# Optimization experiments

Hardware: AMD Instinct MI355X
Metric: run time of the kernel (lower is better)

Reference implementation:

```python
import jax, jax.numpy as jnp
import numpy as np

N_NODES = 500000
EMB = 32
K = 10          # sampled neighbors per node (num_sample in source)
BATCH = 100000


def setup_inputs() -> dict:
    key = jax.random.key(0)
    k1, k2, k3, k4, k5 = jax.random.split(key, 5)
    # xavier-ish scale for weights [emb, 2*emb]
    w_scale = jnp.sqrt(2.0 / (EMB + 2 * EMB)).astype(jnp.float32)
    emb = jax.random.normal(k1, (N_NODES, EMB), dtype=jnp.float32)
    W1 = jax.random.normal(k2, (EMB, 2 * EMB), dtype=jnp.float32) * w_scale
    W2 = jax.random.normal(k3, (EMB, 2 * EMB), dtype=jnp.float32) * w_scale
    node_batch = jax.random.randint(k4, (BATCH,), 0, N_NODES)
    neigh = jax.random.randint(k5, (N_NODES, K), 0, N_NODES)
    return {"emb": emb, "W1": W1, "W2": W2,
            "node_batch": node_batch, "neigh": neigh}


def _sage_layer(self_feat, agg_feat, W):
    # SageLayer.forward: relu(W.mm(cat([self, agg], 1).t()).t()) == relu(cat @ W.T)
    combined = jnp.concatenate([self_feat, agg_feat], axis=1)  # [n, 2E]
    return jax.nn.relu(combined @ W.T)                          # [n, E]


def reference(emb, W1, W2, node_batch, neigh):
    # Layer 1: MEAN aggregation of K sampled neighbors for every node
    # (mask.mm(embed_matrix) with row-normalized 0/1 mask == gather + mean)
    agg1 = jnp.take(emb, neigh, axis=0).mean(axis=1)   # [N, E]
    h1 = _sage_layer(emb, agg1, W1)                    # [N, E]
    # Layer 2: aggregate over neighbors of the batch nodes using layer-1 embeds
    nb_neigh = jnp.take(neigh, node_batch, axis=0)     # [B, K]
    agg2 = jnp.take(h1, nb_neigh, axis=0).mean(axis=1) # [B, E]
    out = _sage_layer(jnp.take(h1, node_batch, axis=0), agg2, W2)  # [B, E]
    return out
```

## Files before the change

kernel.cpp:

```cpp
#include <hip/hip_runtime.h>

#define EMBD 32
#define KN 10

__device__ __forceinline__ float bf2f(unsigned short u) {
    union { unsigned int u; float f; } c; c.u = ((unsigned int)u) << 16; return c.f;
}
__device__ __forceinline__ unsigned short f2bf(float f) {
    union { float f; unsigned int u; } c; c.f = f;
    unsigned int u = c.u + 0x7FFFu + ((c.u >> 16) & 1u);
    return (unsigned short)(u >> 16);
}

__global__ __launch_bounds__(256)
void cvt_bf16_kernel(const float4* __restrict__ in, ushort4* __restrict__ out, int n4)
{
    int i = blockIdx.x * 256 + threadIdx.x;
    if (i < n4) {
        float4 v = in[i];
        ushort4 o;
        o.x = f2bf(v.x); o.y = f2bf(v.y); o.z = f2bf(v.z); o.w = f2bf(v.w);
        out[i] = o;
    }
}

template<bool REMAP, bool OUT_BF16>
__global__ __launch_bounds__(256, 4)
void sage_layer(const unsigned short* __restrict__ feat,
                const float* __restrict__ W,
                const int*   __restrict__ neigh,
                const int*   __restrict__ remap,
                void*        __restrict__ out,
                int n_rows)
{
    __shared__ float sh[64][65];
    __shared__ int   s_nb[64][KN];
    __shared__ int   s_node[64];

    const int tid  = threadIdx.x;
    const int row0 = blockIdx.x << 6;

    if constexpr (REMAP) {
        if (tid < 64) {
            int r = row0 + tid;
            if (r >= n_rows) r = n_rows - 1;
            s_node[tid] = remap[r];
        }
        __syncthreads();
    }

    #pragma unroll
    for (int e = tid; e < 64 * KN; e += 256) {
        const int rl = e / KN;
        const int k  = e - rl * KN;
        int node;
        if constexpr (REMAP) {
            node = s_node[rl];
        } else {
            int r = row0 + rl;
            node = (r >= n_rows) ? n_rows - 1 : r;
        }
        s_nb[rl][k] = neigh[node * KN + k];
    }
    __syncthreads();

    {
        const int hw = tid >> 5;
        const int j  = tid & 31;
        #pragma unroll 2
        for (int i = 0; i < 8; ++i) {
            const int rl = hw * 8 + i;
            int node;
            if constexpr (REMAP) {
                node = s_node[rl];
            } else {
                int r = row0 + rl;
                node = (r >= n_rows) ? n_rows - 1 : r;
            }
            const float self = bf2f(feat[node * EMBD + j]);
            float agg = 0.f;
            #pragma unroll
            for (int k = 0; k < KN; ++k)
                agg += bf2f(feat[s_nb[rl][k] * EMBD + j]);
            sh[j][rl]      = self;
            sh[32 + j][rl] = agg * 0.1f;
        }
    }
    __syncthreads();

    const int row = tid & 63;
    const int wid = __builtin_amdgcn_readfirstlane(tid >> 6);
    const float* Wb = W + wid * 8 * 64;

    float acc[8] = {0.f,0.f,0.f,0.f,0.f,0.f,0.f,0.f};
    #pragma unroll 8
    for (int jj = 0; jj < 64; ++jj) {
        const float c = sh[jj][row];
        #pragma unroll
        for (int q = 0; q < 8; ++q)
            acc[q] = fmaf(c, Wb[q * 64 + jj], acc[q]);
    }

    const int r = row0 + row;
    if (r < n_rows) {
        if (OUT_BF16) {
            unsigned int pk[4];
            #pragma unroll
            for (int q = 0; q < 4; ++q) {
                float a0 = fmaxf(acc[2*q],     0.f);
                float a1 = fmaxf(acc[2*q + 1], 0.f);
                pk[q] = (unsigned int)f2bf(a0) | ((unsigned int)f2bf(a1) << 16);
            }
            uint4* dst = (uint4*)((unsigned short*)out + (size_t)r * EMBD + wid * 8);
            *dst = make_uint4(pk[0], pk[1], pk[2], pk[3]);
        } else {
            float* dst = (float*)out + (size_t)r * EMBD + wid * 8;
            ((float4*)dst)[0] = make_float4(fmaxf(acc[0],0.f), fmaxf(acc[1],0.f),
                                            fmaxf(acc[2],0.f), fmaxf(acc[3],0.f));
            ((float4*)dst)[1] = make_float4(fmaxf(acc[4],0.f), fmaxf(acc[5],0.f),
                                            fmaxf(acc[6],0.f), fmaxf(acc[7],0.f));
        }
    }
}

extern "C" void kernel_launch(void* const* d_in, const int* in_sizes, int n_in,
                              void* d_out, int out_size, void* d_ws, size_t ws_size,
                              hipStream_t stream)
{
    const float* emb        = (const float*)d_in[0];
    const float* W1         = (const float*)d_in[1];
    const float* W2         = (const float*)d_in[2];
    const int*   node_batch = (const int*)  d_in[3];
    const int*   neigh      = (const int*)  d_in[4];

    const int N = in_sizes[0] / EMBD;
    const int B = in_sizes[3];

    unsigned short* emb_bf = (unsigned short*)d_ws;
    unsigned short* h1_bf  = emb_bf + (size_t)N * EMBD;

    const int n4 = (N * EMBD) / 4;
    cvt_bf16_kernel<<<(n4 + 255) / 256, 256, 0, stream>>>(
        (const float4*)emb, (ushort4*)emb_bf, n4);

    sage_layer<false, true><<<(N + 63) / 64, 256, 0, stream>>>(
        emb_bf, W1, neigh, nullptr, (void*)h1_bf, N);

    sage_layer<true, false><<<(B + 63) / 64, 256, 0, stream>>>(
        h1_bf, W2, neigh, node_batch, d_out, B);
}
```

Baseline: 232.5 us.

## Split fused SAGE layer into separate gather and GEMM-ReLU kernels

The single kernel that gathered the neighbor mean and did the small GEMM is replaced by two kernels. The first, agg_gather, runs at higher occupancy (launch bounds 256, 8) and writes the bf16 neighbor mean to a workspace buffer. The second, gemm_relu, reads the self features and the stored aggregate and applies W and ReLU. Layer-1 output is written in place over the bf16 embedding buffer. The aim is better latency hiding for the random gathers, at the cost of an extra round trip of the aggregate through global memory, two more launches, and extra bf16 rounding of the aggregate.

```diff
diff --git a/kernel.cpp b/kernel.cpp
--- a/kernel.cpp
+++ b/kernel.cpp
@@ -24,19 +24,16 @@
     }
 }
 
-template<bool REMAP, bool OUT_BF16>
-__global__ __launch_bounds__(256, 4)
-void sage_layer(const unsigned short* __restrict__ feat,
-                const float* __restrict__ W,
-                const int*   __restrict__ neigh,
-                const int*   __restrict__ remap,
-                void*        __restrict__ out,
+template<bool REMAP>
+__global__ __launch_bounds__(256, 8)
+void agg_gather(const unsigned short* __restrict__ feat,
+                const int*            __restrict__ neigh,
+                const int*            __restrict__ remap,
+                unsigned short*       __restrict__ aggout,
                 int n_rows)
 {
-    __shared__ float sh[64][65];
-    __shared__ int   s_nb[64][KN];
-    __shared__ int   s_node[64];
-
+    __shared__ int s_nb[64][KN];
+    __shared__ int s_node[64];
     const int tid  = threadIdx.x;
     const int row0 = blockIdx.x << 6;
 
@@ -54,15 +51,49 @@
         const int rl = e / KN;
         const int k  = e - rl * KN;
         int node;
-        if constexpr (REMAP) {
-            node = s_node[rl];
-        } else {
-            int r = row0 + rl;
-            node = (r >= n_rows) ? n_rows - 1 : r;
-        }
+        if constexpr (REMAP) node = s_node[rl];
+        else { int r = row0 + rl; node = (r >= n_rows) ? n_rows - 1 : r; }
         s_nb[rl][k] = neigh[node * KN + k];
     }
     __syncthreads();
+
+    const int hw = tid >> 5;
+    const int j  = tid & 31;
+    #pragma unroll 2
+    for (int i = 0; i < 8; ++i) {
+        const int rl = hw * 8 + i;
+        const int r  = row0 + rl;
+        float agg = 0.f;
+        #pragma unroll
+        for (int k = 0; k < KN; ++k)
+            agg += bf2f(feat[s_nb[rl][k] * EMBD + j]);
+        if (r < n_rows)
+            aggout[r * EMBD + j] = f2bf(agg * 0.1f);
+    }
+}
+
+template<bool SELF_REMAP, bool OUT_BF16>
+__global__ __launch_bounds__(256, 4)
+void gemm_relu(const unsigned short* __restrict__ selff,
+               const unsigned short* __restrict__ agg,
+               const float*          __restrict__ W,
+               const int*            __restrict__ remap,
+               void*                 __restrict__ out,
+               int n_rows)
+{
+    __shared__ float sh[64][65];
+    __shared__ int   s_node[64];
+    const int tid  = threadIdx.x;
+    const int row0 = blockIdx.x << 6;
+
+    if constexpr (SELF_REMAP) {
+        if (tid < 64) {
+            int r = row0 + tid;
+            if (r >= n_rows) r = n_rows - 1;
+            s_node[tid] = remap[r];
+        }
+        __syncthreads();
+    }
 
     {
         const int hw = tid >> 5;
@@ -70,20 +101,11 @@
         #pragma unroll 2
         for (int i = 0; i < 8; ++i) {
             const int rl = hw * 8 + i;
-            int node;
-            if constexpr (REMAP) {
-                node = s_node[rl];
-            } else {
-                int r = row0 + rl;
-                node = (r >= n_rows) ? n_rows - 1 : r;
-            }
-            const float self = bf2f(feat[node * EMBD + j]);
-            float agg = 0.f;
-            #pragma unroll
-            for (int k = 0; k < KN; ++k)
-                agg += bf2f(feat[s_nb[rl][k] * EMBD + j]);
-            sh[j][rl]      = self;
-            sh[32 + j][rl] = agg * 0.1f;
+            int r = row0 + rl;
+            if (r >= n_rows) r = n_rows - 1;
+            const int node = SELF_REMAP ? s_node[rl] : r;
+            sh[j][rl]      = bf2f(selff[node * EMBD + j]);
+            sh[32 + j][rl] = bf2f(agg[r * EMBD + j]);
         }
     }
     __syncthreads();
@@ -137,15 +159,19 @@
     const int B = in_sizes[3];
 
     unsigned short* emb_bf = (unsigned short*)d_ws;
-    unsigned short* h1_bf  = emb_bf + (size_t)N * EMBD;
+    unsigned short* agg_bf = emb_bf + (size_t)N * EMBD;
 
     const int n4 = (N * EMBD) / 4;
     cvt_bf16_kernel<<<(n4 + 255) / 256, 256, 0, stream>>>(
         (const float4*)emb, (ushort4*)emb_bf, n4);
 
-    sage_layer<false, true><<<(N + 63) / 64, 256, 0, stream>>>(
-        emb_bf, W1, neigh, nullptr, (void*)h1_bf, N);
+    agg_gather<false><<<(N + 63) / 64, 256, 0, stream>>>(
+        emb_bf, neigh, nullptr, agg_bf, N);
+    gemm_relu<false, true><<<(N + 63) / 64, 256, 0, stream>>>(
+        emb_bf, agg_bf, W1, nullptr, (void*)emb_bf , N);
 
-    sage_layer<true, false><<<(B + 63) / 64, 256, 0, stream>>>(
-        h1_bf, W2, neigh, node_batch, d_out, B);
+    agg_gather<true><<<(B + 63) / 64, 256, 0, stream>>>(
+        emb_bf , neigh, node_batch, agg_bf, B);
+    gemm_relu<true, false><<<(B + 63) / 64, 256, 0, stream>>>(
+        emb_bf , agg_bf, W2, node_batch, d_out, B);
 }
```

New measurement: 275.8 us. 18.7% more time.

## Fuse three launches into one persistent kernel with software grid barriers

Applied to the files above, without the earlier changes.

Replaces the conversion kernel and the two layer kernels with a single persistent kernel of fixed grid size. Blocks grid-stride over conversion work and then over layer tiles, separated by an atomic-counter grid barrier. This removes two launch gaps and kernel tail effects. It relies on all blocks being co-resident (256 CUs at 6 blocks each covers 1536), otherwise the barrier deadlocks, and the barrier spin plus reduced per-tile parallelism may add cost.

```diff
diff --git a/kernel.cpp b/kernel.cpp
--- a/kernel.cpp
+++ b/kernel.cpp
@@ -2,6 +2,10 @@
 
 #define EMBD 32
 #define KN 10
+#define NBLK 1536
+
+__device__ unsigned int g_cnt   = 0;
+__device__ unsigned int g_epoch = 0;
 
 __device__ __forceinline__ float bf2f(unsigned short u) {
     union { unsigned int u; float f; } c; c.u = ((unsigned int)u) << 16; return c.f;
@@ -12,33 +16,45 @@
     return (unsigned short)(u >> 16);
 }
 
-__global__ __launch_bounds__(256)
-void cvt_bf16_kernel(const float4* __restrict__ in, ushort4* __restrict__ out, int n4)
-{
-    int i = blockIdx.x * 256 + threadIdx.x;
-    if (i < n4) {
-        float4 v = in[i];
-        ushort4 o;
-        o.x = f2bf(v.x); o.y = f2bf(v.y); o.z = f2bf(v.z); o.w = f2bf(v.w);
-        out[i] = o;
+__device__ __forceinline__ void gbar() {
+    __syncthreads();
+    if (threadIdx.x == 0) {
+        __threadfence();
+        unsigned int e = __hip_atomic_load(&g_epoch, __ATOMIC_RELAXED,
+                                           __HIP_MEMORY_SCOPE_AGENT);
+        unsigned int a = __hip_atomic_fetch_add(&g_cnt, 1u, __ATOMIC_ACQ_REL,
+                                                __HIP_MEMORY_SCOPE_AGENT);
+        if (a == gridDim.x - 1) {
+            __hip_atomic_store(&g_cnt, 0u, __ATOMIC_RELAXED,
+                               __HIP_MEMORY_SCOPE_AGENT);
+            __hip_atomic_fetch_add(&g_epoch, 1u, __ATOMIC_RELEASE,
+                                   __HIP_MEMORY_SCOPE_AGENT);
+        } else {
+            while (__hip_atomic_load(&g_epoch, __ATOMIC_ACQUIRE,
+                                     __HIP_MEMORY_SCOPE_AGENT) == e)
+                __builtin_amdgcn_s_sleep(8);
+        }
+        __threadfence();
     }
+    __syncthreads();
 }
 
 template<bool REMAP, bool OUT_BF16>
-__global__ __launch_bounds__(256, 4)
-void sage_layer(const unsigned short* __restrict__ feat,
-                const float* __restrict__ W,
-                const int*   __restrict__ neigh,
-                const int*   __restrict__ remap,
-                void*        __restrict__ out,
-                int n_rows)
+__device__ __forceinline__ void sage_tile(
+    const unsigned short* __restrict__ feat,
+    const float*          __restrict__ W,
+    const int*            __restrict__ neigh,
+    const int*            __restrict__ remap,
+    void*                 __restrict__ out,
+    int n_rows, int tile,
+    float (* __restrict__ sh)[65],
+    int   (* __restrict__ s_nb)[KN],
+    int*     __restrict__ s_node)
 {
-    __shared__ float sh[64][65];
-    __shared__ int   s_nb[64][KN];
-    __shared__ int   s_node[64];
+    const int tid  = threadIdx.x;
+    const int row0 = tile << 6;
 
-    const int tid  = threadIdx.x;
-    const int row0 = blockIdx.x << 6;
+    __syncthreads();
 
     if constexpr (REMAP) {
         if (tid < 64) {
@@ -54,12 +70,8 @@
         const int rl = e / KN;
         const int k  = e - rl * KN;
         int node;
-        if constexpr (REMAP) {
-            node = s_node[rl];
-        } else {
-            int r = row0 + rl;
-            node = (r >= n_rows) ? n_rows - 1 : r;
-        }
+        if constexpr (REMAP) node = s_node[rl];
+        else { int r = row0 + rl; node = (r >= n_rows) ? n_rows - 1 : r; }
         s_nb[rl][k] = neigh[node * KN + k];
     }
     __syncthreads();
@@ -71,12 +83,8 @@
         for (int i = 0; i < 8; ++i) {
             const int rl = hw * 8 + i;
             int node;
-            if constexpr (REMAP) {
-                node = s_node[rl];
-            } else {
-                int r = row0 + rl;
-                node = (r >= n_rows) ? n_rows - 1 : r;
-            }
+            if constexpr (REMAP) node = s_node[rl];
+            else { int r = row0 + rl; node = (r >= n_rows) ? n_rows - 1 : r; }
             const float self = bf2f(feat[node * EMBD + j]);
             float agg = 0.f;
             #pragma unroll
@@ -103,7 +111,7 @@
 
     const int r = row0 + row;
     if (r < n_rows) {
-        if (OUT_BF16) {
+        if constexpr (OUT_BF16) {
             unsigned int pk[4];
             #pragma unroll
             for (int q = 0; q < 4; ++q) {
@@ -123,6 +131,51 @@
     }
 }
 
+__global__ __launch_bounds__(256, 6)
+void sage_all(const float4* __restrict__ emb4,
+              const float*  __restrict__ W1,
+              const float*  __restrict__ W2,
+              const int*    __restrict__ node_batch,
+              const int*    __restrict__ neigh,
+              unsigned short* __restrict__ emb_bf,
+              unsigned short* __restrict__ h1_bf,
+              float*        __restrict__ out,
+              int N, int B)
+{
+    __shared__ float sh[64][65];
+    __shared__ int   s_nb[64][KN];
+    __shared__ int   s_node[64];
+
+    const int tid = threadIdx.x;
+
+    {
+        ushort4* ob = (ushort4*)emb_bf;
+        const int n4 = N * (EMBD / 4);
+        for (int i = blockIdx.x * 256 + tid; i < n4; i += gridDim.x * 256) {
+            float4 v = emb4[i];
+            ushort4 o;
+            o.x = f2bf(v.x); o.y = f2bf(v.y); o.z = f2bf(v.z); o.w = f2bf(v.w);
+            ob[i] = o;
+        }
+    }
+    gbar();
+
+    {
+        const int nt = (N + 63) >> 6;
+        for (int t = blockIdx.x; t < nt; t += gridDim.x)
+            sage_tile<false, true>(emb_bf, W1, neigh, nullptr,
+                                   (void*)h1_bf, N, t, sh, s_nb, s_node);
+    }
+    gbar();
+
+    {
+        const int nt = (B + 63) >> 6;
+        for (int t = blockIdx.x; t < nt; t += gridDim.x)
+            sage_tile<true, false>(h1_bf, W2, neigh, node_batch,
+                                   (void*)out, B, t, sh, s_nb, s_node);
+    }
+}
+
 extern "C" void kernel_launch(void* const* d_in, const int* in_sizes, int n_in,
                               void* d_out, int out_size, void* d_ws, size_t ws_size,
                               hipStream_t stream)
@@ -139,13 +192,7 @@
     unsigned short* emb_bf = (unsigned short*)d_ws;
     unsigned short* h1_bf  = emb_bf + (size_t)N * EMBD;
 
-    const int n4 = (N * EMBD) / 4;
-    cvt_bf16_kernel<<<(n4 + 255) / 256, 256, 0, stream>>>(
-        (const float4*)emb, (ushort4*)emb_bf, n4);
-
-    sage_layer<false, true><<<(N + 63) / 64, 256, 0, stream>>>(
-        emb_bf, W1, neigh, nullptr, (void*)h1_bf, N);
-
-    sage_layer<true, false><<<(B + 63) / 64, 256, 0, stream>>>(
-        h1_bf, W2, neigh, node_batch, d_out, B);
+    sage_all<<<NBLK, 256, 0, stream>>>(
+        (const float4*)emb, W1, W2, node_batch, neigh,
+        emb_bf, h1_bf, (float*)d_out, N, B);
 }
```

Result: slower. 898.4 us (+286.5%).
